# Kernel tuning notes

Measured on AMD Instinct MI355X. Metric: run time of the kernel, lower is better.

The kernel has to match this reference:

```python
import jax, jax.numpy as jnp
import numpy as np

NUM_STEPS = 30
LOSS_SCALE = 0.01   # up_loss_fn_scale
LAMBDA0 = 0.1
EPS_DAMP = 1e-6
ATOL = 1e-8
RTOL = 1e-8
LAMB_MIN, LAMB_MAX = 1e-6, 100.0

B, M, N = 32, 307200, 4


def setup_inputs() -> dict:
    key = jax.random.key(0)
    k1, k2, k3, k4 = jax.random.split(key, 4)
    J = jax.random.normal(k1, (B, M, N), dtype=jnp.float32)
    b = jax.random.normal(k2, (B, M), dtype=jnp.float32)
    conf = jax.random.uniform(k3, (B, M), dtype=jnp.float32)
    theta0 = jax.random.normal(k4, (B, N), dtype=jnp.float32)
    return {"J": J, "b": b, "conf": conf, "theta0": theta0}


def huber_loss(x):
    # classical Huber with first derivative (second deriv unused for GN weights)
    mask = x <= 1.0
    sx = jnp.sqrt(x + 1e-8)
    isx = jnp.maximum(jnp.asarray(np.finfo(np.float32).eps, x.dtype), 1.0 / sx)
    loss = jnp.where(mask, x, 2.0 * sx - 1.0)
    loss_d1 = jnp.where(mask, jnp.ones_like(x), isx)
    return loss, loss_d1


def scaled_huber(x, a):
    a2 = a * a
    loss, d1 = huber_loss(x / a2)
    return loss * a2, d1


def reference(J, b, conf, theta0):
    """Batched Levenberg-Marquardt with Huber IRLS weights, damped Cholesky solve,
    lambda update and early-stop masking (device-resident control flow)."""
    nparam = J.shape[-1]
    eye = jnp.eye(nparam, dtype=J.dtype)

    def residual_cost_weight(theta):
        r = b - jnp.einsum('bmn,bn->bm', J, theta)            # (B, M)
        cost, w = scaled_huber(r * r, LOSS_SCALE)
        cost = cost * conf                                     # confidence-weighted cost
        w = w * conf                                           # IRLS weights
        return r, cost.sum(axis=-1), w

    _, cost0, _ = residual_cost_weight(theta0)
    lamb0 = jnp.full((theta0.shape[0],), LAMBDA0, dtype=J.dtype)
    stop0 = jnp.zeros((theta0.shape[0],), dtype=bool)

    def step(carry, _):
        theta, lamb, prev_cost, stop = carry
        r, _, w = residual_cost_weight(theta)
        Jw = J * w[..., None]
        H = jnp.einsum('bmn,bmk->bnk', Jw, J)                  # (B, N, N)
        G = jnp.einsum('bmn,bm->bn', Jw, r)                    # (B, N)
        # LM damping: H += diag_embed(clamp(lambda * diag(H), eps))
        diag = jnp.diagonal(H, axis1=-2, axis2=-1) * lamb[:, None]
        Hd = H + eye * jnp.clip(diag, EPS_DAMP, None)[:, None, :]
        # batched Cholesky solve: Hd delta = G
        L = jnp.linalg.cholesky(Hd)
        y = jax.lax.linalg.triangular_solve(L, G[..., None], left_side=True, lower=True)
        delta = jax.lax.linalg.triangular_solve(L, y, left_side=True, lower=True, transpose_a=True)[..., 0]
        new_theta = theta + delta
        _, new_cost, _ = residual_cost_weight(new_theta)
        # update_lambda
        new_lamb = jnp.clip(lamb * jnp.where(new_cost > prev_cost, 10.0, 0.1), LAMB_MIN, LAMB_MAX)
        # early stop (allclose-style, per batch element), freeze converged entries
        converged = jnp.abs(new_cost - prev_cost) <= ATOL + RTOL * jnp.abs(prev_cost)
        theta = jnp.where(stop[:, None], theta, new_theta)
        lamb = jnp.where(stop, lamb, new_lamb)
        cost = jnp.where(stop, prev_cost, new_cost)
        stop = stop | converged
        return (theta, lamb, cost, stop), None

    (theta, lamb, cost, _), _ = jax.lax.scan(step, (theta0, lamb0, cost0, stop0), None, length=NUM_STEPS)
    return theta, cost
```

## Files before the change

### kernel.cpp

```cpp
#include <hip/hip_runtime.h>
#include <hip/hip_fp16.h>
#include <math.h>


#define B_   32
#define M_   307200
#define M2_  153600
#define NSTEPS 30
#define CHUNKS 32
#define THREADS 256
#define STRIDE  (CHUNKS * THREADS)
#define STRIDE2 (CHUNKS * THREADS)

#define WS_THETA 0
#define WS_EVAL  128
#define WS_LAMB  256
#define WS_COST  288
#define WS_STOP  320
#define WS_PART  352

#define J16_OFF  131072ull
#define B16_OFF  78774272ull
#define C16_OFF  98435072ull
#define WS_NEED  118095872ull

__global__ void lm_init(float* __restrict__ ws, const float* __restrict__ theta0) {
    int i = threadIdx.x;
    if (i < 128) {
        float t = theta0[i];
        ws[WS_THETA + i] = t;
        ws[WS_EVAL + i]  = t;
    }
    if (i < 32) {
        ws[WS_LAMB + i] = 0.1f;
        ws[WS_COST + i] = 0.0f;
        ((int*)(ws + WS_STOP))[i] = 0;
    }
}

__global__ __launch_bounds__(256) void lm_convert(
        const float* __restrict__ J, const float* __restrict__ bvec,
        const float* __restrict__ conf, __half* __restrict__ J16,
        __half* __restrict__ B16, __half* __restrict__ C16) {
    const int total = B_ * (M_ / 2);
    const float4* J4 = (const float4*)J;
    const float2* b2 = (const float2*)bvec;
    const float2* c2 = (const float2*)conf;
    for (int p = blockIdx.x * blockDim.x + threadIdx.x; p < total;
         p += gridDim.x * blockDim.x) {
        float4 a = J4[2 * p];
        float4 c = J4[2 * p + 1];
        __half2* jo = (__half2*)(J16 + (size_t)p * 8);
        jo[0] = __floats2half2_rn(a.x, a.y);
        jo[1] = __floats2half2_rn(a.z, a.w);
        jo[2] = __floats2half2_rn(c.x, c.y);
        jo[3] = __floats2half2_rn(c.z, c.w);
        float2 bv = b2[p];
        ((__half2*)B16)[p] = __floats2half2_rn(bv.x, bv.y);
        float2 cf = c2[p];
        ((__half2*)C16)[p] = __floats2half2_rn(cf.x, cf.y);
    }
}

#define ACC_ROW(jx, jy, jz, jw, bv, cf) do {                          \
    float pred = (jx) * t0 + (jy) * t1 + (jz) * t2 + (jw) * t3;       \
    float r = (bv) - pred;                                            \
    float x  = r * r * 1.0e4f;                                        \
    float sx = sqrtf(x + 1e-8f);                                      \
    float isx = fmaxf(1.1920929e-7f, 1.0f / sx);                      \
    bool small_ = (x <= 1.0f);                                        \
    float loss = small_ ? x : (2.0f * sx - 1.0f);                     \
    float d1   = small_ ? 1.0f : isx;                                 \
    c_acc += loss * 1.0e-4f * (cf);                                   \
    float w  = d1 * (cf);                                             \
    float wr = w * r;                                                 \
    g0 += wr * (jx); g1 += wr * (jy); g2 += wr * (jz); g3 += wr * (jw); \
    float wx = w * (jx), wy = w * (jy), wz = w * (jz);                \
    h00 += wx * (jx); h01 += wx * (jy); h02 += wx * (jz); h03 += wx * (jw); \
    h11 += wy * (jy); h12 += wy * (jz); h13 += wy * (jw);             \
    h22 += wz * (jz); h23 += wz * (jw);                               \
    h33 += (w * (jw)) * (jw);                                         \
} while (0)

#define REDUCE_AND_EMIT() do {                                        \
    float acc[15] = {c_acc, g0, g1, g2, g3,                           \
                     h00, h01, h02, h03, h11, h12, h13, h22, h23, h33}; \
    _Pragma("unroll")                                                 \
    for (int v = 0; v < 15; ++v) {                                    \
        float s = acc[v];                                             \
        _Pragma("unroll")                                             \
        for (int off = 32; off > 0; off >>= 1)                        \
            s += __shfl_down(s, off, 64);                             \
        acc[v] = s;                                                   \
    }                                                                 \
    __shared__ float red[4][15];                                      \
    const int lane = threadIdx.x & 63;                                \
    const int wave = threadIdx.x >> 6;                                \
    if (lane == 0) {                                                  \
        _Pragma("unroll")                                             \
        for (int v = 0; v < 15; ++v) red[wave][v] = acc[v];           \
    }                                                                 \
    __syncthreads();                                                  \
    if (threadIdx.x < 15) {                                           \
        int v = threadIdx.x;                                          \
        float s = red[0][v] + red[1][v] + red[2][v] + red[3][v];      \
        ws[WS_PART + (batch * CHUNKS + chunk) * 16 + v] = s;          \
    }                                                                 \
} while (0)

__global__ __launch_bounds__(THREADS) void lm_pass_f32(
        const float* __restrict__ J, const float* __restrict__ bvec,
        const float* __restrict__ conf, float* __restrict__ ws) {
    const int batch = blockIdx.x & (B_ - 1);
    const int chunk = blockIdx.x >> 5;

    const int* stopf = (const int*)(ws + WS_STOP);
    if (stopf[batch]) return;

    const float* th = ws + WS_EVAL + batch * 4;
    const float t0 = th[0], t1 = th[1], t2 = th[2], t3 = th[3];

    const float4* Jb = (const float4*)(J + (size_t)batch * M_ * 4);
    const float*  bb = bvec + (size_t)batch * M_;
    const float*  cb = conf + (size_t)batch * M_;

    float c_acc = 0.f;
    float g0 = 0.f, g1 = 0.f, g2 = 0.f, g3 = 0.f;
    float h00 = 0.f, h01 = 0.f, h02 = 0.f, h03 = 0.f;
    float h11 = 0.f, h12 = 0.f, h13 = 0.f;
    float h22 = 0.f, h23 = 0.f, h33 = 0.f;

    for (int m = chunk * THREADS + (int)threadIdx.x; m < M_; m += STRIDE) {
        float4 jv = Jb[m];
        float  bv = bb[m];
        float  cf = cb[m];
        ACC_ROW(jv.x, jv.y, jv.z, jv.w, bv, cf);
    }
    REDUCE_AND_EMIT();
}

__global__ __launch_bounds__(THREADS) void lm_pass_f16(
        const __half* __restrict__ J16, const __half* __restrict__ B16,
        const __half* __restrict__ C16, float* __restrict__ ws) {
    const int batch = blockIdx.x & (B_ - 1);
    const int chunk = blockIdx.x >> 5;

    const int* stopf = (const int*)(ws + WS_STOP);
    if (stopf[batch]) return;

    const float* th = ws + WS_EVAL + batch * 4;
    const float t0 = th[0], t1 = th[1], t2 = th[2], t3 = th[3];

    const __half2* Jh = (const __half2*)(J16 + (size_t)batch * M_ * 4);
    const __half2* Bh = (const __half2*)(B16 + (size_t)batch * M_);
    const __half2* Ch = (const __half2*)(C16 + (size_t)batch * M_);

    float c_acc = 0.f;
    float g0 = 0.f, g1 = 0.f, g2 = 0.f, g3 = 0.f;
    float h00 = 0.f, h01 = 0.f, h02 = 0.f, h03 = 0.f;
    float h11 = 0.f, h12 = 0.f, h13 = 0.f;
    float h22 = 0.f, h23 = 0.f, h33 = 0.f;

    for (int i = chunk * THREADS + (int)threadIdx.x; i < M2_; i += STRIDE2) {
        __half2 j01a = Jh[4 * i + 0];
        __half2 j23a = Jh[4 * i + 1];
        __half2 j01b = Jh[4 * i + 2];
        __half2 j23b = Jh[4 * i + 3];
        __half2 bh = Bh[i];
        __half2 ch = Ch[i];
        {
            float jx = __low2float(j01a), jy = __high2float(j01a);
            float jz = __low2float(j23a), jw = __high2float(j23a);
            float bv = __low2float(bh),   cf = __low2float(ch);
            ACC_ROW(jx, jy, jz, jw, bv, cf);
        }
        {
            float jx = __low2float(j01b), jy = __high2float(j01b);
            float jz = __low2float(j23b), jw = __high2float(j23b);
            float bv = __high2float(bh),  cf = __high2float(ch);
            ACC_ROW(jx, jy, jz, jw, bv, cf);
        }
    }
    REDUCE_AND_EMIT();
}

__global__ __launch_bounds__(64) void lm_solve(
        float* __restrict__ ws, float* __restrict__ out, int j) {
    const int batch = blockIdx.x;
    const int tid = threadIdx.x;
    float* theta = ws + WS_THETA + batch * 4;
    float* evalt = ws + WS_EVAL + batch * 4;
    float* lambp = ws + WS_LAMB + batch;
    float* costp = ws + WS_COST + batch;
    int*   stopp = (int*)(ws + WS_STOP) + batch;
    const float* part = ws + WS_PART + batch * CHUNKS * 16;

    __shared__ float vals[15];
    const bool stopped = (*stopp != 0);

    if (!stopped) {
        if (tid < 15) {
            float s = 0.f;
            #pragma unroll 4
            for (int k = 0; k < CHUNKS; ++k) s += part[k * 16 + tid];
            vals[tid] = s;
        }
        __syncthreads();
        if (tid == 0) {
            float new_cost = vals[0];
            float l = *lambp;
            bool stop_now = false;
            if (j == 0) {
                *costp = new_cost;
            } else {
                float prev = *costp;
                float nl = l * (new_cost > prev ? 10.0f : 0.1f);
                nl = fminf(fmaxf(nl, 1e-6f), 100.0f);
                stop_now = fabsf(new_cost - prev) <= (1e-8f + 1e-8f * fabsf(prev));
                theta[0] = evalt[0]; theta[1] = evalt[1];
                theta[2] = evalt[2]; theta[3] = evalt[3];
                *costp = new_cost;
                *lambp = nl;
                l = nl;
                if (stop_now) *stopp = 1;
            }
            if (!stop_now && j < NSTEPS) {
                float g0 = vals[1], g1 = vals[2], g2 = vals[3], g3 = vals[4];
                float a00 = vals[5],  a01 = vals[6],  a02 = vals[7], a03 = vals[8];
                float a11 = vals[9],  a12 = vals[10], a13 = vals[11];
                float a22 = vals[12], a23 = vals[13], a33 = vals[14];
                a00 += fmaxf(l * a00, 1e-6f);
                a11 += fmaxf(l * a11, 1e-6f);
                a22 += fmaxf(l * a22, 1e-6f);
                a33 += fmaxf(l * a33, 1e-6f);
                float L00 = sqrtf(a00);
                float L10 = a01 / L00, L20 = a02 / L00, L30 = a03 / L00;
                float L11 = sqrtf(a11 - L10 * L10);
                float L21 = (a12 - L20 * L10) / L11;
                float L31 = (a13 - L30 * L10) / L11;
                float L22 = sqrtf(a22 - L20 * L20 - L21 * L21);
                float L32 = (a23 - L30 * L20 - L31 * L21) / L22;
                float L33 = sqrtf(a33 - L30 * L30 - L31 * L31 - L32 * L32);
                float y0 = g0 / L00;
                float y1 = (g1 - L10 * y0) / L11;
                float y2 = (g2 - L20 * y0 - L21 * y1) / L22;
                float y3 = (g3 - L30 * y0 - L31 * y1 - L32 * y2) / L33;
                float d3 = y3 / L33;
                float d2 = (y2 - L32 * d3) / L22;
                float d1 = (y1 - L21 * d2 - L31 * d3) / L11;
                float d0 = (y0 - L10 * d1 - L20 * d2 - L30 * d3) / L00;
                evalt[0] = theta[0] + d0;
                evalt[1] = theta[1] + d1;
                evalt[2] = theta[2] + d2;
                evalt[3] = theta[3] + d3;
            }
        }
    }

    if (j == NSTEPS) {
        __syncthreads();
        if (tid < 4)       out[batch * 4 + tid] = theta[tid];
        else if (tid == 4) out[B_ * 4 + batch]  = *costp;
    }
}

extern "C" void kernel_launch(void* const* d_in, const int* in_sizes, int n_in,
                              void* d_out, int out_size, void* d_ws, size_t ws_size,
                              hipStream_t stream) {
    const float* J      = (const float*)d_in[0];
    const float* bvec   = (const float*)d_in[1];
    const float* conf   = (const float*)d_in[2];
    const float* theta0 = (const float*)d_in[3];
    float* ws  = (float*)d_ws;
    float* out = (float*)d_out;

    const bool f16 = (ws_size >= WS_NEED);
    __half* J16 = (__half*)((char*)d_ws + J16_OFF);
    __half* B16 = (__half*)((char*)d_ws + B16_OFF);
    __half* C16 = (__half*)((char*)d_ws + C16_OFF);

    hipLaunchKernelGGL(lm_init, dim3(1), dim3(128), 0, stream, ws, theta0);
    if (f16) {
        hipLaunchKernelGGL(lm_convert, dim3(2048), dim3(256), 0, stream,
                           J, bvec, conf, J16, B16, C16);
    }
    for (int j = 0; j <= NSTEPS; ++j) {
        if (f16) {
            hipLaunchKernelGGL(lm_pass_f16, dim3(B_ * CHUNKS), dim3(THREADS), 0,
                               stream, J16, B16, C16, ws);
        } else {
            hipLaunchKernelGGL(lm_pass_f32, dim3(B_ * CHUNKS), dim3(THREADS), 0,
                               stream, J, bvec, conf, ws);
        }
        hipLaunchKernelGGL(lm_solve, dim3(B_), dim3(64), 0, stream, ws, out, j);
    }
}
```

Before: 1.226 ms.

## Fuse fp16 conversion into first pass and solve into each pass kernel

The fp32-to-fp16 conversion now happens inside the first accumulation pass, so J, b and conf are read once instead of twice. The per-step solve kernel is folded into the start of the next pass: every block redundantly reduces the partials and does the 4x4 Cholesky, with double-buffered control state indexed by step parity. This removes 31 small solve launches and one full read of the inputs, at the cost of redundant per-block solve work and a serial prologue before each streaming pass. The workspace layout also changes, and a final small kernel writes the outputs.

```diff
diff --git a/kernel.cpp b/kernel.cpp
--- a/kernel.cpp
+++ b/kernel.cpp
@@ -12,55 +12,25 @@
 #define STRIDE  (CHUNKS * THREADS)
 #define STRIDE2 (CHUNKS * THREADS)
 
+#define C_TH 0
+#define C_EV 256
+#define C_LA 512
+#define C_CO 576
+#define C_SP 640
+#define C_PT 704
+
+#define J16_OFF  0ull
+#define B16_OFF  78643200ull
+#define C16_OFF  98304000ull
+#define CTRL_OFF 117964800ull
+#define WS_NEED  (CTRL_OFF + 133888ull)
+
 #define WS_THETA 0
 #define WS_EVAL  128
 #define WS_LAMB  256
 #define WS_COST  288
 #define WS_STOP  320
 #define WS_PART  352
-
-#define J16_OFF  131072ull
-#define B16_OFF  78774272ull
-#define C16_OFF  98435072ull
-#define WS_NEED  118095872ull
-
-__global__ void lm_init(float* __restrict__ ws, const float* __restrict__ theta0) {
-    int i = threadIdx.x;
-    if (i < 128) {
-        float t = theta0[i];
-        ws[WS_THETA + i] = t;
-        ws[WS_EVAL + i]  = t;
-    }
-    if (i < 32) {
-        ws[WS_LAMB + i] = 0.1f;
-        ws[WS_COST + i] = 0.0f;
-        ((int*)(ws + WS_STOP))[i] = 0;
-    }
-}
-
-__global__ __launch_bounds__(256) void lm_convert(
-        const float* __restrict__ J, const float* __restrict__ bvec,
-        const float* __restrict__ conf, __half* __restrict__ J16,
-        __half* __restrict__ B16, __half* __restrict__ C16) {
-    const int total = B_ * (M_ / 2);
-    const float4* J4 = (const float4*)J;
-    const float2* b2 = (const float2*)bvec;
-    const float2* c2 = (const float2*)conf;
-    for (int p = blockIdx.x * blockDim.x + threadIdx.x; p < total;
-         p += gridDim.x * blockDim.x) {
-        float4 a = J4[2 * p];
-        float4 c = J4[2 * p + 1];
-        __half2* jo = (__half2*)(J16 + (size_t)p * 8);
-        jo[0] = __floats2half2_rn(a.x, a.y);
-        jo[1] = __floats2half2_rn(a.z, a.w);
-        jo[2] = __floats2half2_rn(c.x, c.y);
-        jo[3] = __floats2half2_rn(c.z, c.w);
-        float2 bv = b2[p];
-        ((__half2*)B16)[p] = __floats2half2_rn(bv.x, bv.y);
-        float2 cf = c2[p];
-        ((__half2*)C16)[p] = __floats2half2_rn(cf.x, cf.y);
-    }
-}
 
 #define ACC_ROW(jx, jy, jz, jw, bv, cf) do {                          \
     float pred = (jx) * t0 + (jy) * t1 + (jz) * t2 + (jw) * t3;       \
@@ -82,7 +52,7 @@
     h33 += (w * (jw)) * (jw);                                         \
 } while (0)
 
-#define REDUCE_AND_EMIT() do {                                        \
+#define REDUCE_AND_EMIT(dst) do {                                     \
     float acc[15] = {c_acc, g0, g1, g2, g3,                           \
                      h00, h01, h02, h03, h11, h12, h13, h22, h23, h33}; \
     _Pragma("unroll")                                                 \
@@ -93,36 +63,56 @@
             s += __shfl_down(s, off, 64);                             \
         acc[v] = s;                                                   \
     }                                                                 \
-    __shared__ float red[4][15];                                      \
-    const int lane = threadIdx.x & 63;                                \
-    const int wave = threadIdx.x >> 6;                                \
-    if (lane == 0) {                                                  \
+    __shared__ float red_[4][15];                                     \
+    const int lane_ = threadIdx.x & 63;                               \
+    const int wave_ = threadIdx.x >> 6;                               \
+    if (lane_ == 0) {                                                 \
         _Pragma("unroll")                                             \
-        for (int v = 0; v < 15; ++v) red[wave][v] = acc[v];           \
+        for (int v = 0; v < 15; ++v) red_[wave_][v] = acc[v];         \
     }                                                                 \
     __syncthreads();                                                  \
     if (threadIdx.x < 15) {                                           \
         int v = threadIdx.x;                                          \
-        float s = red[0][v] + red[1][v] + red[2][v] + red[3][v];      \
-        ws[WS_PART + (batch * CHUNKS + chunk) * 16 + v] = s;          \
+        (dst)[v] = red_[0][v] + red_[1][v] + red_[2][v] + red_[3][v]; \
     }                                                                 \
 } while (0)
 
-__global__ __launch_bounds__(THREADS) void lm_pass_f32(
+
+__global__ void lm_init16(float* __restrict__ ctrl, const float* __restrict__ theta0) {
+    int i = threadIdx.x;
+    if (i < 128) {
+        float t = theta0[i];
+        ctrl[C_TH + i] = t;
+        ctrl[C_EV + i] = t;
+    }
+    if (i < 32) {
+        ctrl[C_LA + i] = 0.1f;
+        ctrl[C_CO + i] = 0.0f;
+        ((int*)(ctrl + C_SP))[i]      = 0;
+        ((int*)(ctrl + C_SP))[32 + i] = 0;
+    }
+}
+
+__global__ __launch_bounds__(THREADS) void lm_pass0(
         const float* __restrict__ J, const float* __restrict__ bvec,
-        const float* __restrict__ conf, float* __restrict__ ws) {
+        const float* __restrict__ conf, float* __restrict__ ctrl,
+        __half* __restrict__ J16, __half* __restrict__ B16,
+        __half* __restrict__ C16) {
     const int batch = blockIdx.x & (B_ - 1);
     const int chunk = blockIdx.x >> 5;
-
-    const int* stopf = (const int*)(ws + WS_STOP);
-    if (stopf[batch]) return;
-
-    const float* th = ws + WS_EVAL + batch * 4;
-    const float t0 = th[0], t1 = th[1], t2 = th[2], t3 = th[3];
-
-    const float4* Jb = (const float4*)(J + (size_t)batch * M_ * 4);
-    const float*  bb = bvec + (size_t)batch * M_;
-    const float*  cb = conf + (size_t)batch * M_;
+    const int tid   = threadIdx.x;
+
+    const float t0 = ctrl[C_EV + batch * 4 + 0];
+    const float t1 = ctrl[C_EV + batch * 4 + 1];
+    const float t2 = ctrl[C_EV + batch * 4 + 2];
+    const float t3 = ctrl[C_EV + batch * 4 + 3];
+
+    const float4* J4 = (const float4*)(J + (size_t)batch * M_ * 4);
+    const float2* b2 = (const float2*)(bvec + (size_t)batch * M_);
+    const float2* c2 = (const float2*)(conf + (size_t)batch * M_);
+    __half2* Jh = (__half2*)(J16 + (size_t)batch * M_ * 4);
+    __half2* Bh = (__half2*)(B16 + (size_t)batch * M_);
+    __half2* Ch = (__half2*)(C16 + (size_t)batch * M_);
 
     float c_acc = 0.f;
     float g0 = 0.f, g1 = 0.f, g2 = 0.f, g3 = 0.f;
@@ -130,26 +120,130 @@
     float h11 = 0.f, h12 = 0.f, h13 = 0.f;
     float h22 = 0.f, h23 = 0.f, h33 = 0.f;
 
-    for (int m = chunk * THREADS + (int)threadIdx.x; m < M_; m += STRIDE) {
-        float4 jv = Jb[m];
-        float  bv = bb[m];
-        float  cf = cb[m];
-        ACC_ROW(jv.x, jv.y, jv.z, jv.w, bv, cf);
-    }
-    REDUCE_AND_EMIT();
+    for (int p = chunk * THREADS + tid; p < M2_; p += STRIDE2) {
+        float4 a = J4[2 * p];
+        float4 c = J4[2 * p + 1];
+        float2 bv = b2[p];
+        float2 cf = c2[p];
+        ACC_ROW(a.x, a.y, a.z, a.w, bv.x, cf.x);
+        ACC_ROW(c.x, c.y, c.z, c.w, bv.y, cf.y);
+        Jh[4 * p + 0] = __floats2half2_rn(a.x, a.y);
+        Jh[4 * p + 1] = __floats2half2_rn(a.z, a.w);
+        Jh[4 * p + 2] = __floats2half2_rn(c.x, c.y);
+        Jh[4 * p + 3] = __floats2half2_rn(c.z, c.w);
+        Bh[p] = __floats2half2_rn(bv.x, bv.y);
+        Ch[p] = __floats2half2_rn(cf.x, cf.y);
+    }
+
+    float* dst = ctrl + C_PT + (batch * CHUNKS + chunk) * 16;
+    REDUCE_AND_EMIT(dst);
 }
 
 __global__ __launch_bounds__(THREADS) void lm_pass_f16(
         const __half* __restrict__ J16, const __half* __restrict__ B16,
-        const __half* __restrict__ C16, float* __restrict__ ws) {
+        const __half* __restrict__ C16, float* __restrict__ ctrl, int j) {
     const int batch = blockIdx.x & (B_ - 1);
     const int chunk = blockIdx.x >> 5;
-
-    const int* stopf = (const int*)(ws + WS_STOP);
-    if (stopf[batch]) return;
-
-    const float* th = ws + WS_EVAL + batch * 4;
-    const float t0 = th[0], t1 = th[1], t2 = th[2], t3 = th[3];
+    const int tid   = threadIdx.x;
+    const int pr = (j - 1) & 1;
+    const int cu = j & 1;
+
+    int* sp = (int*)(ctrl + C_SP);
+    if (sp[pr * 32 + batch]) {
+        if (chunk == 0 && tid == 0) {
+            #pragma unroll
+            for (int i = 0; i < 4; ++i)
+                ctrl[C_TH + cu * 128 + batch * 4 + i] =
+                    ctrl[C_TH + pr * 128 + batch * 4 + i];
+            ctrl[C_CO + cu * 32 + batch] = ctrl[C_CO + pr * 32 + batch];
+            sp[cu * 32 + batch] = 1;
+        }
+        return;
+    }
+
+    __shared__ float vals[15];
+    __shared__ float sev[4];
+    __shared__ int   srun;
+
+    const float* pt = ctrl + C_PT + pr * 16384 + batch * CHUNKS * 16;
+    if (tid < 15) {
+        float s = 0.f;
+        #pragma unroll 8
+        for (int k = 0; k < CHUNKS; ++k) s += pt[k * 16 + tid];
+        vals[tid] = s;
+    }
+    __syncthreads();
+
+    if (tid == 0) {
+        float new_cost = vals[0];
+        float l, thc0, thc1, thc2, thc3;
+        bool stop_now = false;
+        if (j == 1) {
+            l = ctrl[C_LA + pr * 32 + batch];
+            thc0 = ctrl[C_TH + pr * 128 + batch * 4 + 0];
+            thc1 = ctrl[C_TH + pr * 128 + batch * 4 + 1];
+            thc2 = ctrl[C_TH + pr * 128 + batch * 4 + 2];
+            thc3 = ctrl[C_TH + pr * 128 + batch * 4 + 3];
+        } else {
+            float prev = ctrl[C_CO + pr * 32 + batch];
+            l = ctrl[C_LA + pr * 32 + batch];
+            float nl = l * (new_cost > prev ? 10.0f : 0.1f);
+            nl = fminf(fmaxf(nl, 1e-6f), 100.0f);
+            stop_now = fabsf(new_cost - prev) <= (1e-8f + 1e-8f * fabsf(prev));
+            thc0 = ctrl[C_EV + pr * 128 + batch * 4 + 0];
+            thc1 = ctrl[C_EV + pr * 128 + batch * 4 + 1];
+            thc2 = ctrl[C_EV + pr * 128 + batch * 4 + 2];
+            thc3 = ctrl[C_EV + pr * 128 + batch * 4 + 3];
+            l = nl;
+        }
+        if (chunk == 0) {
+            ctrl[C_TH + cu * 128 + batch * 4 + 0] = thc0;
+            ctrl[C_TH + cu * 128 + batch * 4 + 1] = thc1;
+            ctrl[C_TH + cu * 128 + batch * 4 + 2] = thc2;
+            ctrl[C_TH + cu * 128 + batch * 4 + 3] = thc3;
+            ctrl[C_CO + cu * 32 + batch] = new_cost;
+            ctrl[C_LA + cu * 32 + batch] = l;
+            sp[cu * 32 + batch] = stop_now ? 1 : 0;
+        }
+        if (!stop_now) {
+            float g0 = vals[1], g1 = vals[2], g2 = vals[3], g3 = vals[4];
+            float a00 = vals[5],  a01 = vals[6],  a02 = vals[7], a03 = vals[8];
+            float a11 = vals[9],  a12 = vals[10], a13 = vals[11];
+            float a22 = vals[12], a23 = vals[13], a33 = vals[14];
+            a00 += fmaxf(l * a00, 1e-6f);
+            a11 += fmaxf(l * a11, 1e-6f);
+            a22 += fmaxf(l * a22, 1e-6f);
+            a33 += fmaxf(l * a33, 1e-6f);
+            float L00 = sqrtf(a00);
+            float L10 = a01 / L00, L20 = a02 / L00, L30 = a03 / L00;
+            float L11 = sqrtf(a11 - L10 * L10);
+            float L21 = (a12 - L20 * L10) / L11;
+            float L31 = (a13 - L30 * L10) / L11;
+            float L22 = sqrtf(a22 - L20 * L20 - L21 * L21);
+            float L32 = (a23 - L30 * L20 - L31 * L21) / L22;
+            float L33 = sqrtf(a33 - L30 * L30 - L31 * L31 - L32 * L32);
+            float y0 = g0 / L00;
+            float y1 = (g1 - L10 * y0) / L11;
+            float y2 = (g2 - L20 * y0 - L21 * y1) / L22;
+            float y3 = (g3 - L30 * y0 - L31 * y1 - L32 * y2) / L33;
+            float d3 = y3 / L33;
+            float d2 = (y2 - L32 * d3) / L22;
+            float d1 = (y1 - L21 * d2 - L31 * d3) / L11;
+            float d0 = (y0 - L10 * d1 - L20 * d2 - L30 * d3) / L00;
+            sev[0] = thc0 + d0; sev[1] = thc1 + d1;
+            sev[2] = thc2 + d2; sev[3] = thc3 + d3;
+            if (chunk == 0) {
+                ctrl[C_EV + cu * 128 + batch * 4 + 0] = sev[0];
+                ctrl[C_EV + cu * 128 + batch * 4 + 1] = sev[1];
+                ctrl[C_EV + cu * 128 + batch * 4 + 2] = sev[2];
+                ctrl[C_EV + cu * 128 + batch * 4 + 3] = sev[3];
+            }
+        }
+        srun = stop_now ? 0 : 1;
+    }
+    __syncthreads();
+    if (!srun) return;
+    const float t0 = sev[0], t1 = sev[1], t2 = sev[2], t3 = sev[3];
 
     const __half2* Jh = (const __half2*)(J16 + (size_t)batch * M_ * 4);
     const __half2* Bh = (const __half2*)(B16 + (size_t)batch * M_);
@@ -161,7 +255,7 @@
     float h11 = 0.f, h12 = 0.f, h13 = 0.f;
     float h22 = 0.f, h23 = 0.f, h33 = 0.f;
 
-    for (int i = chunk * THREADS + (int)threadIdx.x; i < M2_; i += STRIDE2) {
+    for (int i = chunk * THREADS + tid; i < M2_; i += STRIDE2) {
         __half2 j01a = Jh[4 * i + 0];
         __half2 j23a = Jh[4 * i + 1];
         __half2 j01b = Jh[4 * i + 2];
@@ -181,7 +275,81 @@
             ACC_ROW(jx, jy, jz, jw, bv, cf);
         }
     }
-    REDUCE_AND_EMIT();
+
+    float* dst = ctrl + C_PT + cu * 16384 + (batch * CHUNKS + chunk) * 16;
+    REDUCE_AND_EMIT(dst);
+}
+
+__global__ __launch_bounds__(64) void lm_finalize16(
+        const float* __restrict__ ctrl, float* __restrict__ out) {
+    const int batch = blockIdx.x;
+    const int tid = threadIdx.x;
+    const int pr = NSTEPS & 1;
+
+    const int* sp = (const int*)(ctrl + C_SP);
+    if (sp[pr * 32 + batch]) {
+        if (tid < 4)       out[batch * 4 + tid] = ctrl[C_TH + pr * 128 + batch * 4 + tid];
+        else if (tid == 4) out[B_ * 4 + batch]  = ctrl[C_CO + pr * 32 + batch];
+        return;
+    }
+    __shared__ float vals[15];
+    const float* pt = ctrl + C_PT + pr * 16384 + batch * CHUNKS * 16;
+    if (tid < 15) {
+        float s = 0.f;
+        #pragma unroll 8
+        for (int k = 0; k < CHUNKS; ++k) s += pt[k * 16 + tid];
+        vals[tid] = s;
+    }
+    __syncthreads();
+    if (tid < 4)       out[batch * 4 + tid] = ctrl[C_EV + pr * 128 + batch * 4 + tid];
+    else if (tid == 4) out[B_ * 4 + batch]  = vals[0];
+}
+
+
+__global__ void lm_init(float* __restrict__ ws, const float* __restrict__ theta0) {
+    int i = threadIdx.x;
+    if (i < 128) {
+        float t = theta0[i];
+        ws[WS_THETA + i] = t;
+        ws[WS_EVAL + i]  = t;
+    }
+    if (i < 32) {
+        ws[WS_LAMB + i] = 0.1f;
+        ws[WS_COST + i] = 0.0f;
+        ((int*)(ws + WS_STOP))[i] = 0;
+    }
+}
+
+__global__ __launch_bounds__(THREADS) void lm_pass_f32(
+        const float* __restrict__ J, const float* __restrict__ bvec,
+        const float* __restrict__ conf, float* __restrict__ ws) {
+    const int batch = blockIdx.x & (B_ - 1);
+    const int chunk = blockIdx.x >> 5;
+
+    const int* stopf = (const int*)(ws + WS_STOP);
+    if (stopf[batch]) return;
+
+    const float* th = ws + WS_EVAL + batch * 4;
+    const float t0 = th[0], t1 = th[1], t2 = th[2], t3 = th[3];
+
+    const float4* Jb = (const float4*)(J + (size_t)batch * M_ * 4);
+    const float*  bb = bvec + (size_t)batch * M_;
+    const float*  cb = conf + (size_t)batch * M_;
+
+    float c_acc = 0.f;
+    float g0 = 0.f, g1 = 0.f, g2 = 0.f, g3 = 0.f;
+    float h00 = 0.f, h01 = 0.f, h02 = 0.f, h03 = 0.f;
+    float h11 = 0.f, h12 = 0.f, h13 = 0.f;
+    float h22 = 0.f, h23 = 0.f, h33 = 0.f;
+
+    for (int m = chunk * THREADS + (int)threadIdx.x; m < M_; m += STRIDE) {
+        float4 jv = Jb[m];
+        float  bv = bb[m];
+        float  cf = cb[m];
+        ACC_ROW(jv.x, jv.y, jv.z, jv.w, bv, cf);
+    }
+    float* dst = ws + WS_PART + (batch * CHUNKS + chunk) * 16;
+    REDUCE_AND_EMIT(dst);
 }
 
 __global__ __launch_bounds__(64) void lm_solve(
@@ -264,6 +432,7 @@
     }
 }
 
+
 extern "C" void kernel_launch(void* const* d_in, const int* in_sizes, int n_in,
                               void* d_out, int out_size, void* d_ws, size_t ws_size,
                               hipStream_t stream) {
@@ -271,27 +440,29 @@
     const float* bvec   = (const float*)d_in[1];
     const float* conf   = (const float*)d_in[2];
     const float* theta0 = (const float*)d_in[3];
-    float* ws  = (float*)d_ws;
     float* out = (float*)d_out;
 
-    const bool f16 = (ws_size >= WS_NEED);
-    __half* J16 = (__half*)((char*)d_ws + J16_OFF);
-    __half* B16 = (__half*)((char*)d_ws + B16_OFF);
-    __half* C16 = (__half*)((char*)d_ws + C16_OFF);
-
-    hipLaunchKernelGGL(lm_init, dim3(1), dim3(128), 0, stream, ws, theta0);
-    if (f16) {
-        hipLaunchKernelGGL(lm_convert, dim3(2048), dim3(256), 0, stream,
-                           J, bvec, conf, J16, B16, C16);
-    }
-    for (int j = 0; j <= NSTEPS; ++j) {
-        if (f16) {
+    if (ws_size >= WS_NEED) {
+        __half* J16 = (__half*)((char*)d_ws + J16_OFF);
+        __half* B16 = (__half*)((char*)d_ws + B16_OFF);
+        __half* C16 = (__half*)((char*)d_ws + C16_OFF);
+        float*  ctrl = (float*)((char*)d_ws + CTRL_OFF);
+
+        hipLaunchKernelGGL(lm_init16, dim3(1), dim3(128), 0, stream, ctrl, theta0);
+        hipLaunchKernelGGL(lm_pass0, dim3(B_ * CHUNKS), dim3(THREADS), 0, stream,
+                           J, bvec, conf, ctrl, J16, B16, C16);
+        for (int j = 1; j <= NSTEPS; ++j) {
             hipLaunchKernelGGL(lm_pass_f16, dim3(B_ * CHUNKS), dim3(THREADS), 0,
-                               stream, J16, B16, C16, ws);
-        } else {
+                               stream, J16, B16, C16, ctrl, j);
+        }
+        hipLaunchKernelGGL(lm_finalize16, dim3(B_), dim3(64), 0, stream, ctrl, out);
+    } else {
+        float* ws = (float*)d_ws;
+        hipLaunchKernelGGL(lm_init, dim3(1), dim3(128), 0, stream, ws, theta0);
+        for (int j = 0; j <= NSTEPS; ++j) {
             hipLaunchKernelGGL(lm_pass_f32, dim3(B_ * CHUNKS), dim3(THREADS), 0,
                                stream, J, bvec, conf, ws);
-        }
-        hipLaunchKernelGGL(lm_solve, dim3(B_), dim3(64), 0, stream, ws, out, j);
-    }
-}
+            hipLaunchKernelGGL(lm_solve, dim3(B_), dim3(64), 0, stream, ws, out, j);
+        }
+    }
+}
```

Result: faster. 1.120 ms (-8.7%).
